# Performance work log

Measured on AMD Instinct MI355X. Metric: run time of the kernel, lower is better.

The kernel has to match this reference:

```python
import jax, jax.numpy as jnp
import numpy as np

TEMP = 0.2
M, K, B = 8192, 128, 100


def setup_inputs() -> dict:
    key = jax.random.key(0)
    k1, k2, k3 = jax.random.split(key, 3)
    f = jax.random.normal(k1, (M, K), dtype=jnp.float32)
    features = f / jnp.linalg.norm(f, axis=1, keepdims=True)
    p = jax.random.normal(k2, (B, K), dtype=jnp.float32)
    protos = p / jnp.linalg.norm(p, axis=1, keepdims=True)
    labels = jax.random.randint(k3, (M,), 0, 2 * B, dtype=jnp.int32)
    proto_labels = jnp.arange(B, dtype=jnp.int32)
    return {"features": features, "labels": labels, "protos": protos, "proto_labels": proto_labels}


def reference(features, labels, protos, proto_labels):
    m = features.shape[0]
    dt = features.dtype
    # base = samples whose label appears among prototype labels
    base = (labels[None, :] == proto_labels[:, None]).any(axis=0)  # [M] bool
    novel = ~base
    nf = novel.astype(dt)
    bf = base.astype(dt)

    S = jnp.matmul(features, features.T) / TEMP          # [M, M] sample-sample logits
    P = jnp.matmul(features, protos.T) / TEMP            # [M, B] sample-proto logits

    # novel-novel pair mask: both novel, off-diagonal (fill_diagonal_(0))
    pair = nf[:, None] * nf[None, :] * (1.0 - jnp.eye(m, dtype=dt))  # [M, M]
    expS = jnp.exp(S)

    # --- novel loss (note: original adds RAW ni_pk.sum, not exp -- faithful) ---
    exp_sum = (expS * pair).sum(axis=1)                  # sum_{j novel, j!=i} exp(S_ij)
    denom = exp_sum + P.sum(axis=1)                      # + raw proto logit sum
    safe_den = jnp.where(novel, denom, 1.0)
    cnt = pair.sum(axis=1)                               # novel_label_mask is all-True 1D -> just pair count
    safe_cnt = jnp.where(cnt > 0, cnt, 1.0)
    # sum_j pair_ij * (S_ij - log(den_i)) = (S*pair).sum - log(den)*cnt
    num = (S * pair).sum(axis=1) - jnp.log(safe_den) * cnt
    loss_novel = (-(num / safe_cnt) * nf).sum()

    # --- base loss ---
    safe_lab = jnp.where(base, labels, 0)
    bi_pi = jnp.take_along_axis(P, safe_lab[:, None], axis=1)[:, 0]  # P[i, labels[i]]
    exp_nk = (expS * nf[None, :]).sum(axis=1)            # sum over novel columns
    exp_pk = jnp.exp(P).sum(axis=1)
    loss_base = (-(bi_pi - jnp.log(exp_nk + exp_pk)) * bf).sum()

    return (loss_novel + loss_base) / m
```

## Files before the change

kernel.cpp:

```cpp
#include <hip/hip_runtime.h>
#include <stdint.h>


#define M_TOT 8192
#define K_DIM 128
#define B_PRO 100
#define INV_T 5.0f
#define C_SCALE 7.2134752044448170f
#define LN2    0.6931471805599453f
#define RT    256
#define NT    (M_TOT / RT)
#define NPAIR (NT * (NT - 1) / 2)
#define NBLK  (NT + NPAIR)
#define BS    136
#define PB    112

#if __has_builtin(__builtin_amdgcn_exp2f)
#define EXP2(x) __builtin_amdgcn_exp2f(x)
#else
#define EXP2(x) __expf((x) * 0.6931471805599453f)
#endif

typedef __attribute__((ext_vector_type(8))) short  short8;
typedef __attribute__((ext_vector_type(4))) float  floatx4;

__device__ __forceinline__ float bf2f(unsigned short u) {
    union { unsigned int i; float f; } v; v.i = ((unsigned int)u) << 16; return v.f;
}
__device__ __forceinline__ unsigned short f2bf(float x) {
    union { float f; unsigned int i; } v; v.f = x;
    return (unsigned short)((v.i + 0x7fffu + ((v.i >> 16) & 1u)) >> 16);
}
__device__ __forceinline__ short8 pack8(float4 a, float4 b) {
    short8 r;
    r[0] = (short)f2bf(a.x); r[1] = (short)f2bf(a.y);
    r[2] = (short)f2bf(a.z); r[3] = (short)f2bf(a.w);
    r[4] = (short)f2bf(b.x); r[5] = (short)f2bf(b.y);
    r[6] = (short)f2bf(b.z); r[7] = (short)f2bf(b.w);
    return r;
}

template<bool DIAG>
__device__ __forceinline__ void sym_body(
        int a, int b, int R0, int C0,
        const float* __restrict__ feat, const int* __restrict__ labels,
        const float* __restrict__ protos, const int* __restrict__ plabels,
        float* __restrict__ rowE,
        int* __restrict__ nfpart, int* __restrict__ nf,
        float* __restrict__ Psum, float* __restrict__ expPsum,
        float* __restrict__ PLab, float* __restrict__ gpart,
        unsigned short* ldsB, float (*colE)[256],
        float* novR, float* novC, int* plabL, int* labRow, float* redD) {
    const int tid = threadIdx.x;
    const int wv = tid >> 6, lane = tid & 63;
    const int quad = lane >> 4, cq = lane & 15;

    if (tid < B_PRO) plabL[tid] = plabels[tid];

    short8 afr[2][4];
    #pragma unroll
    for (int mt = 0; mt < 2; ++mt)
        #pragma unroll
        for (int ks = 0; ks < 4; ++ks) {
            const float* s = feat + (size_t)(R0 + wv * 32 + mt * 16 + cq) * K_DIM
                             + ks * 32 + quad * 8;
            float4 x = ((const float4*)s)[0];
            float4 y = ((const float4*)s)[1];
            afr[mt][ks] = pack8(x, y);
        }
    __syncthreads();

    {
        const int g = (tid < 256) ? (R0 + tid) : (C0 + (tid - 256));
        const int lbl = labels[g];
        int m = 0;
        #pragma unroll 4
        for (int j = 0; j < B_PRO; ++j) m |= (plabL[j] == lbl);
        const float nv = m ? 0.f : 1.f;
        if (tid < 256) { novR[tid] = nv; labRow[tid] = lbl; }
        else novC[tid - 256] = nv;
    }
    __syncthreads();

    float nmR[2][4];
    #pragma unroll
    for (int mt = 0; mt < 2; ++mt)
        #pragma unroll
        for (int r = 0; r < 4; ++r)
            nmR[mt][r] = novR[wv * 32 + mt * 16 + quad * 4 + r];
    float nmcA[16];
    #pragma unroll
    for (int c2 = 0; c2 < 16; ++c2)
        nmcA[c2] = novC[c2 * 16 + cq];

    float accE[2][4];
    #pragma unroll
    for (int mt = 0; mt < 2; ++mt)
        #pragma unroll
        for (int r = 0; r < 4; ++r) accE[mt][r] = 0.f;

    float g_acc = 0.f;

    const int rbase = R0 + wv * 32 + quad * 4;

    #pragma unroll 1
    for (int half = 0; half < 2; ++half) {
        for (int e = tid; e < 2048; e += 512) {
            const int col = e >> 4, sg = e & 15;
            const float* s = feat + (size_t)(C0 + half * 128 + col) * K_DIM + sg * 8;
            float4 x = ((const float4*)s)[0];
            float4 y = ((const float4*)s)[1];
            ushort4 o0 = make_ushort4(f2bf(x.x*C_SCALE), f2bf(x.y*C_SCALE),
                                      f2bf(x.z*C_SCALE), f2bf(x.w*C_SCALE));
            ushort4 o1 = make_ushort4(f2bf(y.x*C_SCALE), f2bf(y.y*C_SCALE),
                                      f2bf(y.z*C_SCALE), f2bf(y.w*C_SCALE));
            *(ushort4*)&ldsB[col * BS + sg * 8]     = o0;
            *(ushort4*)&ldsB[col * BS + sg * 8 + 4] = o1;
        }
        __syncthreads();

        #pragma unroll 2
        for (int ct8 = 0; ct8 < 8; ++ct8) {
            const int ct = half * 8 + ct8;
            const unsigned short* bp = &ldsB[(ct8 * 16 + cq) * BS + quad * 8];
            short8 b0 = *(const short8*)(bp);
            short8 b1 = *(const short8*)(bp + 32);
            short8 b2 = *(const short8*)(bp + 64);
            short8 b3 = *(const short8*)(bp + 96);

            floatx4 D0 = (floatx4){0.f, 0.f, 0.f, 0.f};
            floatx4 D1 = (floatx4){0.f, 0.f, 0.f, 0.f};
            D0 = __builtin_amdgcn_mfma_f32_16x16x32_bf16(afr[0][0], b0, D0, 0, 0, 0);
            D0 = __builtin_amdgcn_mfma_f32_16x16x32_bf16(afr[0][1], b1, D0, 0, 0, 0);
            D0 = __builtin_amdgcn_mfma_f32_16x16x32_bf16(afr[0][2], b2, D0, 0, 0, 0);
            D0 = __builtin_amdgcn_mfma_f32_16x16x32_bf16(afr[0][3], b3, D0, 0, 0, 0);
            D1 = __builtin_amdgcn_mfma_f32_16x16x32_bf16(afr[1][0], b0, D1, 0, 0, 0);
            D1 = __builtin_amdgcn_mfma_f32_16x16x32_bf16(afr[1][1], b1, D1, 0, 0, 0);
            D1 = __builtin_amdgcn_mfma_f32_16x16x32_bf16(afr[1][2], b2, D1, 0, 0, 0);
            D1 = __builtin_amdgcn_mfma_f32_16x16x32_bf16(afr[1][3], b3, D1, 0, 0, 0);

            const float nmc = nmcA[ct];
            float cpE = 0.f;
            #pragma unroll
            for (int r = 0; r < 4; ++r) {
                float e0 = EXP2(D0[r]), e1 = EXP2(D1[r]);
                if (DIAG) {
                    const int colg = C0 + ct * 16 + cq;
                    if (rbase + r == colg) e0 = 0.f;
                    if (rbase + 16 + r == colg) e1 = 0.f;
                }
                accE[0][r] += e0 * nmc;  cpE += e0 * nmR[0][r];
                accE[1][r] += e1 * nmc;  cpE += e1 * nmR[1][r];
            }
            cpE += __shfl_xor(cpE, 16); cpE += __shfl_xor(cpE, 32);
            if (quad == 0) colE[wv][ct * 16 + cq] = cpE;
        }

        if (DIAG && tid < 128) {
            float s = 0.f;
            #pragma unroll 4
            for (int c2 = 0; c2 < 128; ++c2)
                s += novC[half * 128 + c2] * bf2f(ldsB[c2 * BS + tid]);
            g_acc += s;
        }
        __syncthreads();
    }

    #pragma unroll
    for (int mt = 0; mt < 2; ++mt)
        #pragma unroll
        for (int r = 0; r < 4; ++r) {
            float e = accE[mt][r];
            e += __shfl_xor(e, 1); e += __shfl_xor(e, 2);
            e += __shfl_xor(e, 4); e += __shfl_xor(e, 8);
            accE[mt][r] = e;
        }
    if (cq == 0) {
        const size_t slotR = (size_t)b * M_TOT;
        #pragma unroll
        for (int mt = 0; mt < 2; ++mt)
            #pragma unroll
            for (int r = 0; r < 4; ++r) {
                const int rowg = R0 + wv * 32 + mt * 16 + quad * 4 + r;
                rowE[slotR + rowg] = accE[mt][r];
            }
    }

    if (!DIAG) {
        if (tid < 256) {
            float ce = 0.f;
            #pragma unroll
            for (int w = 0; w < 8; ++w) ce += colE[w][tid];
            rowE[(size_t)a * M_TOT + C0 + tid] = ce;
        }
    } else {
        if (tid < 128) gpart[a * 128 + tid] = g_acc;
        {
            float nvv = (tid < 256) ? novR[tid] : 0.f;
            for (int off = 1; off < 64; off <<= 1) nvv += __shfl_xor(nvv, off);
            if (lane == 0) redD[wv] = nvv;
        }
        if (tid < 256) nf[R0 + tid] = (int)novR[tid];

        for (int idx = tid; idx < 3200; idx += 512) {
            const int pr = idx >> 5, sg = idx & 31;
            float4 v = ((const float4*)protos)[idx];
            *(ushort4*)&ldsB[pr * BS + sg * 4] =
                make_ushort4(f2bf(v.x), f2bf(v.y), f2bf(v.z), f2bf(v.w));
        }
        for (int idx = tid; idx < 384; idx += 512) {
            const int pr = B_PRO + (idx >> 5), sg = idx & 31;
            *(ushort4*)&ldsB[pr * BS + sg * 4] = make_ushort4(0, 0, 0, 0);
        }
        __syncthreads();

        if (tid == 0) {
            float c = 0.f;
            #pragma unroll
            for (int w = 0; w < 8; ++w) c += redD[w];
            nfpart[a] = (int)c;
        }

        float ps2[2][4], es2[2][4], pl2[2][4];
        #pragma unroll
        for (int mt = 0; mt < 2; ++mt)
            #pragma unroll
            for (int r = 0; r < 4; ++r) { ps2[mt][r]=0.f; es2[mt][r]=0.f; pl2[mt][r]=0.f; }

        #pragma unroll 1
        for (int g = 0; g < 7; ++g) {
            const unsigned short* bp = &ldsB[(g * 16 + cq) * BS + quad * 8];
            short8 b0 = *(const short8*)(bp);
            short8 b1 = *(const short8*)(bp + 32);
            short8 b2 = *(const short8*)(bp + 64);
            short8 b3 = *(const short8*)(bp + 96);
            floatx4 E0 = (floatx4){0.f, 0.f, 0.f, 0.f};
            floatx4 E1 = (floatx4){0.f, 0.f, 0.f, 0.f};
            E0 = __builtin_amdgcn_mfma_f32_16x16x32_bf16(afr[0][0], b0, E0, 0, 0, 0);
            E0 = __builtin_amdgcn_mfma_f32_16x16x32_bf16(afr[0][1], b1, E0, 0, 0, 0);
            E0 = __builtin_amdgcn_mfma_f32_16x16x32_bf16(afr[0][2], b2, E0, 0, 0, 0);
            E0 = __builtin_amdgcn_mfma_f32_16x16x32_bf16(afr[0][3], b3, E0, 0, 0, 0);
            E1 = __builtin_amdgcn_mfma_f32_16x16x32_bf16(afr[1][0], b0, E1, 0, 0, 0);
            E1 = __builtin_amdgcn_mfma_f32_16x16x32_bf16(afr[1][1], b1, E1, 0, 0, 0);
            E1 = __builtin_amdgcn_mfma_f32_16x16x32_bf16(afr[1][2], b2, E1, 0, 0, 0);
            E1 = __builtin_amdgcn_mfma_f32_16x16x32_bf16(afr[1][3], b3, E1, 0, 0, 0);
            const int bcol = g * 16 + cq;
            if (bcol < B_PRO) {
                #pragma unroll
                for (int r = 0; r < 4; ++r) {
                    const float Pv0 = E0[r] * INV_T;
                    ps2[0][r] += Pv0; es2[0][r] += __expf(Pv0);
                    if (bcol == labRow[wv * 32 + quad * 4 + r]) pl2[0][r] += Pv0;
                    const float Pv1 = E1[r] * INV_T;
                    ps2[1][r] += Pv1; es2[1][r] += __expf(Pv1);
                    if (bcol == labRow[wv * 32 + 16 + quad * 4 + r]) pl2[1][r] += Pv1;
                }
            }
        }
        #pragma unroll
        for (int mt = 0; mt < 2; ++mt)
            #pragma unroll
            for (int r = 0; r < 4; ++r) {
                float p = ps2[mt][r], e = es2[mt][r], l = pl2[mt][r];
                p += __shfl_xor(p, 1); p += __shfl_xor(p, 2);
                p += __shfl_xor(p, 4); p += __shfl_xor(p, 8);
                e += __shfl_xor(e, 1); e += __shfl_xor(e, 2);
                e += __shfl_xor(e, 4); e += __shfl_xor(e, 8);
                l += __shfl_xor(l, 1); l += __shfl_xor(l, 2);
                l += __shfl_xor(l, 4); l += __shfl_xor(l, 8);
                if (cq == 0) {
                    const int rowg = R0 + wv * 32 + mt * 16 + quad * 4 + r;
                    Psum[rowg] = p; expPsum[rowg] = e; PLab[rowg] = l;
                }
            }
    }
}

__global__ __launch_bounds__(512, 4) void k_sym(
        const float* __restrict__ feat, const int* __restrict__ labels,
        const float* __restrict__ protos, const int* __restrict__ plabels,
        float* __restrict__ rowE,
        int* __restrict__ nfpart, int* __restrict__ nf,
        float* __restrict__ Psum, float* __restrict__ expPsum,
        float* __restrict__ PLab, float* __restrict__ gpart,
        float* __restrict__ out) {
    __shared__ unsigned short ldsB[128 * BS];
    __shared__ float colE[8][256];
    __shared__ float novR[256];
    __shared__ float novC[256];
    __shared__ int plabL[B_PRO];
    __shared__ int labRow[256];
    __shared__ float redD[8];

    if (blockIdx.x == 0 && threadIdx.x == 0) out[0] = 0.f;

    const int id = blockIdx.x;
    if (id < NT) {
        sym_body<true>(id, id, id * RT, id * RT,
                       feat, labels, protos, plabels, rowE,
                       nfpart, nf, Psum, expPsum, PLab, gpart,
                       ldsB, colE, novR, novC, plabL, labRow, redD);
    } else {
        const int p = id - NT;
        int aa = 0, rem = p;
        while (rem >= NT - 1 - aa) { rem -= (NT - 1 - aa); ++aa; }
        const int bb2 = aa + 1 + rem;
        sym_body<false>(aa, bb2, aa * RT, bb2 * RT,
                        feat, labels, protos, plabels, rowE,
                        nfpart, nf, Psum, expPsum, PLab, gpart,
                        ldsB, colE, novR, novC, plabL, labRow, redD);
    }
}

__global__ __launch_bounds__(128) void k_final(
        const float* __restrict__ feat,
        const float* __restrict__ rowE,
        const float* __restrict__ Psum, const float* __restrict__ expPsum,
        const float* __restrict__ PLab, const int* __restrict__ nf,
        const int* __restrict__ nfpart, const float* __restrict__ gpart,
        float* __restrict__ out) {
    __shared__ float g[128];
    __shared__ int shNn;
    __shared__ float red[2];
    const int tid = threadIdx.x;
    const int i = blockIdx.x * 128 + tid;

    {
        float s = 0.f;
        #pragma unroll 4
        for (int a2 = 0; a2 < 32; ++a2) s += gpart[a2 * 128 + tid];
        g[tid] = s;
    }
    if (tid < 32) {
        int c = nfpart[tid];
        for (int off = 1; off < 32; off <<= 1) c += __shfl_xor(c, off);
        if (tid == 0) shNn = c;
    }
    __syncthreads();

    float e0 = 0.f, e1 = 0.f, e2 = 0.f, e3 = 0.f;
    #pragma unroll
    for (int s = 0; s < 8; ++s) {
        e0 += rowE[(size_t)(4 * s + 0) * M_TOT + i];
        e1 += rowE[(size_t)(4 * s + 1) * M_TOT + i];
        e2 += rowE[(size_t)(4 * s + 2) * M_TOT + i];
        e3 += rowE[(size_t)(4 * s + 3) * M_TOT + i];
    }
    const float ep = (e0 + e1) + (e2 + e3);

    const float* fr = feat + (size_t)i * K_DIM;
    float sZ = 0.f, dd = 0.f;
    #pragma unroll 8
    for (int k4 = 0; k4 < 32; ++k4) {
        float4 v = ((const float4*)fr)[k4];
        const float fb0 = bf2f(f2bf(v.x)), fc0 = bf2f(f2bf(v.x * C_SCALE));
        const float fb1 = bf2f(f2bf(v.y)), fc1 = bf2f(f2bf(v.y * C_SCALE));
        const float fb2 = bf2f(f2bf(v.z)), fc2 = bf2f(f2bf(v.z * C_SCALE));
        const float fb3 = bf2f(f2bf(v.w)), fc3 = bf2f(f2bf(v.w * C_SCALE));
        const float* gv = &g[k4 * 4];
        sZ += fb0 * gv[0]; dd += fb0 * fc0;
        sZ += fb1 * gv[1]; dd += fb1 * fc1;
        sZ += fb2 * gv[2]; dd += fb2 * fc2;
        sZ += fb3 * gv[3]; dd += fb3 * fc3;
    }

    const int Nn = shNn;
    float contrib;
    if (nf[i]) {
        const float cnt = (float)(Nn - 1);
        const float denom = ep + Psum[i];
        const float sp = sZ - dd;
        const float num = sp * LN2 - logf(denom) * cnt;
        const float sc = cnt > 0.f ? cnt : 1.f;
        contrib = -(num / sc);
    } else {
        contrib = -(PLab[i] - logf(ep + expPsum[i]));
    }
    for (int off = 1; off < 64; off <<= 1) contrib += __shfl_xor(contrib, off);
    if ((tid & 63) == 0) red[tid >> 6] = contrib;
    __syncthreads();
    if (tid == 0) atomicAdd(out, (red[0] + red[1]) * (1.0f / (float)M_TOT));
}

extern "C" void kernel_launch(void* const* d_in, const int* in_sizes, int n_in,
                              void* d_out, int out_size, void* d_ws, size_t ws_size,
                              hipStream_t stream) {
    const float* feat    = (const float*)d_in[0];
    const int*   labels  = (const int*)d_in[1];
    const float* protos  = (const float*)d_in[2];
    const int*   plabels = (const int*)d_in[3];
    float* out = (float*)d_out;

    char* ws = (char*)d_ws;
    float* rowE    = (float*)ws;
    int*   nfpart  = (int*)(ws + 1048576);
    int*   nf      = (int*)(ws + 1052672);
    float* Psum    = (float*)(ws + 1085440);
    float* expPsum = (float*)(ws + 1118208);
    float* PLab    = (float*)(ws + 1150976);
    float* gpart   = (float*)(ws + 1183744);

    k_sym<<<NBLK, 512, 0, stream>>>(feat, labels, protos, plabels,
                                    rowE, nfpart, nf,
                                    Psum, expPsum, PLab, gpart, out);
    k_final<<<64, 128, 0, stream>>>(feat, rowE, Psum, expPsum, PLab,
                                    nf, nfpart, gpart, out);
}
```

Baseline: 102.1 us.

## Split each 256x256 symmetric tile into two 256x128 column-half blocks

Each symmetric tile's work now goes to two blocks, one per 128-column half, instead of one block looping over both halves. This doubles the grid (528 to 1056 blocks) to improve load balance and occupancy across CUs, and removes the in-block serial half loop and its barriers. The cost is that each half-block reloads and repacks the A-row fragments and labels, the rowE and gpart partial buffers double, and k_final must sum twice as many partials. Only the half-0 diagonal blocks compute the prototype logits.

```diff
diff --git a/kernel.cpp b/kernel.cpp
--- a/kernel.cpp
+++ b/kernel.cpp
@@ -11,7 +11,8 @@
 #define RT    256
 #define NT    (M_TOT / RT)
 #define NPAIR (NT * (NT - 1) / 2)
-#define NBLK  (NT + NPAIR)
+#define NTILE (NT + NPAIR)
+#define NBLK  (2 * NTILE)
 #define BS    136
 #define PB    112
 
@@ -42,14 +43,14 @@
 
 template<bool DIAG>
 __device__ __forceinline__ void sym_body(
-        int a, int b, int R0, int C0,
+        int a, int b, int half, int R0, int C0,
         const float* __restrict__ feat, const int* __restrict__ labels,
         const float* __restrict__ protos, const int* __restrict__ plabels,
         float* __restrict__ rowE,
         int* __restrict__ nfpart, int* __restrict__ nf,
         float* __restrict__ Psum, float* __restrict__ expPsum,
         float* __restrict__ PLab, float* __restrict__ gpart,
-        unsigned short* ldsB, float (*colE)[256],
+        unsigned short* ldsB, float (*colE)[128],
         float* novR, float* novC, int* plabL, int* labRow, float* redD) {
     const int tid = threadIdx.x;
     const int wv = tid >> 6, lane = tid & 63;
@@ -68,9 +69,22 @@
             float4 y = ((const float4*)s)[1];
             afr[mt][ks] = pack8(x, y);
         }
+
+    for (int e = tid; e < 2048; e += 512) {
+        const int col = e >> 4, sg = e & 15;
+        const float* s = feat + (size_t)(C0 + col) * K_DIM + sg * 8;
+        float4 x = ((const float4*)s)[0];
+        float4 y = ((const float4*)s)[1];
+        ushort4 o0 = make_ushort4(f2bf(x.x*C_SCALE), f2bf(x.y*C_SCALE),
+                                  f2bf(x.z*C_SCALE), f2bf(x.w*C_SCALE));
+        ushort4 o1 = make_ushort4(f2bf(y.x*C_SCALE), f2bf(y.y*C_SCALE),
+                                  f2bf(y.z*C_SCALE), f2bf(y.w*C_SCALE));
+        *(ushort4*)&ldsB[col * BS + sg * 8]     = o0;
+        *(ushort4*)&ldsB[col * BS + sg * 8 + 4] = o1;
+    }
     __syncthreads();
 
-    {
+    if (tid < 384) {
         const int g = (tid < 256) ? (R0 + tid) : (C0 + (tid - 256));
         const int lbl = labels[g];
         int m = 0;
@@ -88,9 +102,9 @@
         #pragma unroll
         for (int r = 0; r < 4; ++r)
             nmR[mt][r] = novR[wv * 32 + mt * 16 + quad * 4 + r];
-    float nmcA[16];
-    #pragma unroll
-    for (int c2 = 0; c2 < 16; ++c2)
+    float nmcA[8];
+    #pragma unroll
+    for (int c2 = 0; c2 < 8; ++c2)
         nmcA[c2] = novC[c2 * 16 + cq];
 
     float accE[2][4];
@@ -99,71 +113,49 @@
         #pragma unroll
         for (int r = 0; r < 4; ++r) accE[mt][r] = 0.f;
 
+    const int rbase = R0 + wv * 32 + quad * 4;
+
+    #pragma unroll 2
+    for (int ct = 0; ct < 8; ++ct) {
+        const unsigned short* bp = &ldsB[(ct * 16 + cq) * BS + quad * 8];
+        short8 b0 = *(const short8*)(bp);
+        short8 b1 = *(const short8*)(bp + 32);
+        short8 b2 = *(const short8*)(bp + 64);
+        short8 b3 = *(const short8*)(bp + 96);
+
+        floatx4 D0 = (floatx4){0.f, 0.f, 0.f, 0.f};
+        floatx4 D1 = (floatx4){0.f, 0.f, 0.f, 0.f};
+        D0 = __builtin_amdgcn_mfma_f32_16x16x32_bf16(afr[0][0], b0, D0, 0, 0, 0);
+        D0 = __builtin_amdgcn_mfma_f32_16x16x32_bf16(afr[0][1], b1, D0, 0, 0, 0);
+        D0 = __builtin_amdgcn_mfma_f32_16x16x32_bf16(afr[0][2], b2, D0, 0, 0, 0);
+        D0 = __builtin_amdgcn_mfma_f32_16x16x32_bf16(afr[0][3], b3, D0, 0, 0, 0);
+        D1 = __builtin_amdgcn_mfma_f32_16x16x32_bf16(afr[1][0], b0, D1, 0, 0, 0);
+        D1 = __builtin_amdgcn_mfma_f32_16x16x32_bf16(afr[1][1], b1, D1, 0, 0, 0);
+        D1 = __builtin_amdgcn_mfma_f32_16x16x32_bf16(afr[1][2], b2, D1, 0, 0, 0);
+        D1 = __builtin_amdgcn_mfma_f32_16x16x32_bf16(afr[1][3], b3, D1, 0, 0, 0);
+
+        const float nmc = nmcA[ct];
+        float cpE = 0.f;
+        #pragma unroll
+        for (int r = 0; r < 4; ++r) {
+            float e0 = EXP2(D0[r]), e1 = EXP2(D1[r]);
+            if (DIAG) {
+                const int colg = C0 + ct * 16 + cq;
+                if (rbase + r == colg) e0 = 0.f;
+                if (rbase + 16 + r == colg) e1 = 0.f;
+            }
+            accE[0][r] += e0 * nmc;  cpE += e0 * nmR[0][r];
+            accE[1][r] += e1 * nmc;  cpE += e1 * nmR[1][r];
+        }
+        cpE += __shfl_xor(cpE, 16); cpE += __shfl_xor(cpE, 32);
+        if (quad == 0) colE[wv][ct * 16 + cq] = cpE;
+    }
+
     float g_acc = 0.f;
-
-    const int rbase = R0 + wv * 32 + quad * 4;
-
-    #pragma unroll 1
-    for (int half = 0; half < 2; ++half) {
-        for (int e = tid; e < 2048; e += 512) {
-            const int col = e >> 4, sg = e & 15;
-            const float* s = feat + (size_t)(C0 + half * 128 + col) * K_DIM + sg * 8;
-            float4 x = ((const float4*)s)[0];
-            float4 y = ((const float4*)s)[1];
-            ushort4 o0 = make_ushort4(f2bf(x.x*C_SCALE), f2bf(x.y*C_SCALE),
-                                      f2bf(x.z*C_SCALE), f2bf(x.w*C_SCALE));
-            ushort4 o1 = make_ushort4(f2bf(y.x*C_SCALE), f2bf(y.y*C_SCALE),
-                                      f2bf(y.z*C_SCALE), f2bf(y.w*C_SCALE));
-            *(ushort4*)&ldsB[col * BS + sg * 8]     = o0;
-            *(ushort4*)&ldsB[col * BS + sg * 8 + 4] = o1;
-        }
-        __syncthreads();
-
-        #pragma unroll 2
-        for (int ct8 = 0; ct8 < 8; ++ct8) {
-            const int ct = half * 8 + ct8;
-            const unsigned short* bp = &ldsB[(ct8 * 16 + cq) * BS + quad * 8];
-            short8 b0 = *(const short8*)(bp);
-            short8 b1 = *(const short8*)(bp + 32);
-            short8 b2 = *(const short8*)(bp + 64);
-            short8 b3 = *(const short8*)(bp + 96);
-
-            floatx4 D0 = (floatx4){0.f, 0.f, 0.f, 0.f};
-            floatx4 D1 = (floatx4){0.f, 0.f, 0.f, 0.f};
-            D0 = __builtin_amdgcn_mfma_f32_16x16x32_bf16(afr[0][0], b0, D0, 0, 0, 0);
-            D0 = __builtin_amdgcn_mfma_f32_16x16x32_bf16(afr[0][1], b1, D0, 0, 0, 0);
-            D0 = __builtin_amdgcn_mfma_f32_16x16x32_bf16(afr[0][2], b2, D0, 0, 0, 0);
-            D0 = __builtin_amdgcn_mfma_f32_16x16x32_bf16(afr[0][3], b3, D0, 0, 0, 0);
-            D1 = __builtin_amdgcn_mfma_f32_16x16x32_bf16(afr[1][0], b0, D1, 0, 0, 0);
-            D1 = __builtin_amdgcn_mfma_f32_16x16x32_bf16(afr[1][1], b1, D1, 0, 0, 0);
-            D1 = __builtin_amdgcn_mfma_f32_16x16x32_bf16(afr[1][2], b2, D1, 0, 0, 0);
-            D1 = __builtin_amdgcn_mfma_f32_16x16x32_bf16(afr[1][3], b3, D1, 0, 0, 0);
-
-            const float nmc = nmcA[ct];
-            float cpE = 0.f;
-            #pragma unroll
-            for (int r = 0; r < 4; ++r) {
-                float e0 = EXP2(D0[r]), e1 = EXP2(D1[r]);
-                if (DIAG) {
-                    const int colg = C0 + ct * 16 + cq;
-                    if (rbase + r == colg) e0 = 0.f;
-                    if (rbase + 16 + r == colg) e1 = 0.f;
-                }
-                accE[0][r] += e0 * nmc;  cpE += e0 * nmR[0][r];
-                accE[1][r] += e1 * nmc;  cpE += e1 * nmR[1][r];
-            }
-            cpE += __shfl_xor(cpE, 16); cpE += __shfl_xor(cpE, 32);
-            if (quad == 0) colE[wv][ct * 16 + cq] = cpE;
-        }
-
-        if (DIAG && tid < 128) {
-            float s = 0.f;
-            #pragma unroll 4
-            for (int c2 = 0; c2 < 128; ++c2)
-                s += novC[half * 128 + c2] * bf2f(ldsB[c2 * BS + tid]);
-            g_acc += s;
-        }
-        __syncthreads();
+    if (DIAG && tid < 128) {
+        #pragma unroll 4
+        for (int c2 = 0; c2 < 128; ++c2)
+            g_acc += novC[c2] * bf2f(ldsB[c2 * BS + tid]);
     }
 
     #pragma unroll
@@ -176,7 +168,7 @@
             accE[mt][r] = e;
         }
     if (cq == 0) {
-        const size_t slotR = (size_t)b * M_TOT;
+        const size_t slotR = (size_t)(2 * b + half) * M_TOT;
         #pragma unroll
         for (int mt = 0; mt < 2; ++mt)
             #pragma unroll
@@ -186,93 +178,98 @@
             }
     }
 
+    __syncthreads();
+
     if (!DIAG) {
-        if (tid < 256) {
+        if (tid < 128) {
             float ce = 0.f;
             #pragma unroll
             for (int w = 0; w < 8; ++w) ce += colE[w][tid];
-            rowE[(size_t)a * M_TOT + C0 + tid] = ce;
+            rowE[(size_t)(2 * a + half) * M_TOT + C0 + tid] = ce;
         }
     } else {
-        if (tid < 128) gpart[a * 128 + tid] = g_acc;
-        {
-            float nvv = (tid < 256) ? novR[tid] : 0.f;
-            for (int off = 1; off < 64; off <<= 1) nvv += __shfl_xor(nvv, off);
-            if (lane == 0) redD[wv] = nvv;
-        }
-        if (tid < 256) nf[R0 + tid] = (int)novR[tid];
-
-        for (int idx = tid; idx < 3200; idx += 512) {
-            const int pr = idx >> 5, sg = idx & 31;
-            float4 v = ((const float4*)protos)[idx];
-            *(ushort4*)&ldsB[pr * BS + sg * 4] =
-                make_ushort4(f2bf(v.x), f2bf(v.y), f2bf(v.z), f2bf(v.w));
-        }
-        for (int idx = tid; idx < 384; idx += 512) {
-            const int pr = B_PRO + (idx >> 5), sg = idx & 31;
-            *(ushort4*)&ldsB[pr * BS + sg * 4] = make_ushort4(0, 0, 0, 0);
-        }
-        __syncthreads();
-
-        if (tid == 0) {
-            float c = 0.f;
+        if (tid < 128) gpart[(2 * a + half) * 128 + tid] = g_acc;
+
+        if (half == 0) {
+            {
+                float nvv = (tid < 256) ? novR[tid] : 0.f;
+                for (int off = 1; off < 64; off <<= 1) nvv += __shfl_xor(nvv, off);
+                if (lane == 0) redD[wv] = nvv;
+            }
+            if (tid < 256) nf[R0 + tid] = (int)novR[tid];
+
+            for (int idx = tid; idx < 3200; idx += 512) {
+                const int pr = idx >> 5, sg = idx & 31;
+                float4 v = ((const float4*)protos)[idx];
+                *(ushort4*)&ldsB[pr * BS + sg * 4] =
+                    make_ushort4(f2bf(v.x), f2bf(v.y), f2bf(v.z), f2bf(v.w));
+            }
+            for (int idx = tid; idx < 384; idx += 512) {
+                const int pr = B_PRO + (idx >> 5), sg = idx & 31;
+                *(ushort4*)&ldsB[pr * BS + sg * 4] = make_ushort4(0, 0, 0, 0);
+            }
+            __syncthreads();
+
+            if (tid == 0) {
+                float c = 0.f;
+                #pragma unroll
+                for (int w = 0; w < 8; ++w) c += redD[w];
+                nfpart[a] = (int)c;
+            }
+
+            float ps2[2][4], es2[2][4], pl2[2][4];
             #pragma unroll
-            for (int w = 0; w < 8; ++w) c += redD[w];
-            nfpart[a] = (int)c;
-        }
-
-        float ps2[2][4], es2[2][4], pl2[2][4];
-        #pragma unroll
-        for (int mt = 0; mt < 2; ++mt)
+            for (int mt = 0; mt < 2; ++mt)
+                #pragma unroll
+                for (int r = 0; r < 4; ++r) { ps2[mt][r]=0.f; es2[mt][r]=0.f; pl2[mt][r]=0.f; }
+
+            #pragma unroll 1
+            for (int g = 0; g < 7; ++g) {
+                const unsigned short* bp = &ldsB[(g * 16 + cq) * BS + quad * 8];
+                short8 b0 = *(const short8*)(bp);
+                short8 b1 = *(const short8*)(bp + 32);
+                short8 b2 = *(const short8*)(bp + 64);
+                short8 b3 = *(const short8*)(bp + 96);
+                floatx4 E0 = (floatx4){0.f, 0.f, 0.f, 0.f};
+                floatx4 E1 = (floatx4){0.f, 0.f, 0.f, 0.f};
+                E0 = __builtin_amdgcn_mfma_f32_16x16x32_bf16(afr[0][0], b0, E0, 0, 0, 0);
+                E0 = __builtin_amdgcn_mfma_f32_16x16x32_bf16(afr[0][1], b1, E0, 0, 0, 0);
+                E0 = __builtin_amdgcn_mfma_f32_16x16x32_bf16(afr[0][2], b2, E0, 0, 0, 0);
+                E0 = __builtin_amdgcn_mfma_f32_16x16x32_bf16(afr[0][3], b3, E0, 0, 0, 0);
+                E1 = __builtin_amdgcn_mfma_f32_16x16x32_bf16(afr[1][0], b0, E1, 0, 0, 0);
+                E1 = __builtin_amdgcn_mfma_f32_16x16x32_bf16(afr[1][1], b1, E1, 0, 0, 0);
+                E1 = __builtin_amdgcn_mfma_f32_16x16x32_bf16(afr[1][2], b2, E1, 0, 0, 0);
+                E1 = __builtin_amdgcn_mfma_f32_16x16x32_bf16(afr[1][3], b3, E1, 0, 0, 0);
+                const int bcol = g * 16 + cq;
+                if (bcol < B_PRO) {
+                    #pragma unroll
+                    for (int r = 0; r < 4; ++r) {
+                        const float Pv0 = E0[r] * INV_T;
+                        ps2[0][r] += Pv0; es2[0][r] += __expf(Pv0);
+                        if (bcol == labRow[wv * 32 + quad * 4 + r]) pl2[0][r] += Pv0;
+                        const float Pv1 = E1[r] * INV_T;
+                        ps2[1][r] += Pv1; es2[1][r] += __expf(Pv1);
+                        if (bcol == labRow[wv * 32 + 16 + quad * 4 + r]) pl2[1][r] += Pv1;
+                    }
+                }
+            }
             #pragma unroll
-            for (int r = 0; r < 4; ++r) { ps2[mt][r]=0.f; es2[mt][r]=0.f; pl2[mt][r]=0.f; }
-
-        #pragma unroll 1
-        for (int g = 0; g < 7; ++g) {
-            const unsigned short* bp = &ldsB[(g * 16 + cq) * BS + quad * 8];
-            short8 b0 = *(const short8*)(bp);
-            short8 b1 = *(const short8*)(bp + 32);
-            short8 b2 = *(const short8*)(bp + 64);
-            short8 b3 = *(const short8*)(bp + 96);
-            floatx4 E0 = (floatx4){0.f, 0.f, 0.f, 0.f};
-            floatx4 E1 = (floatx4){0.f, 0.f, 0.f, 0.f};
-            E0 = __builtin_amdgcn_mfma_f32_16x16x32_bf16(afr[0][0], b0, E0, 0, 0, 0);
-            E0 = __builtin_amdgcn_mfma_f32_16x16x32_bf16(afr[0][1], b1, E0, 0, 0, 0);
-            E0 = __builtin_amdgcn_mfma_f32_16x16x32_bf16(afr[0][2], b2, E0, 0, 0, 0);
-            E0 = __builtin_amdgcn_mfma_f32_16x16x32_bf16(afr[0][3], b3, E0, 0, 0, 0);
-            E1 = __builtin_amdgcn_mfma_f32_16x16x32_bf16(afr[1][0], b0, E1, 0, 0, 0);
-            E1 = __builtin_amdgcn_mfma_f32_16x16x32_bf16(afr[1][1], b1, E1, 0, 0, 0);
-            E1 = __builtin_amdgcn_mfma_f32_16x16x32_bf16(afr[1][2], b2, E1, 0, 0, 0);
-            E1 = __builtin_amdgcn_mfma_f32_16x16x32_bf16(afr[1][3], b3, E1, 0, 0, 0);
-            const int bcol = g * 16 + cq;
-            if (bcol < B_PRO) {
+            for (int mt = 0; mt < 2; ++mt)
                 #pragma unroll
                 for (int r = 0; r < 4; ++r) {
-                    const float Pv0 = E0[r] * INV_T;
-                    ps2[0][r] += Pv0; es2[0][r] += __expf(Pv0);
-                    if (bcol == labRow[wv * 32 + quad * 4 + r]) pl2[0][r] += Pv0;
-                    const float Pv1 = E1[r] * INV_T;
-                    ps2[1][r] += Pv1; es2[1][r] += __expf(Pv1);
-                    if (bcol == labRow[wv * 32 + 16 + quad * 4 + r]) pl2[1][r] += Pv1;
+                    float p = ps2[mt][r], e = es2[mt][r], l = pl2[mt][r];
+                    p += __shfl_xor(p, 1); p += __shfl_xor(p, 2);
+                    p += __shfl_xor(p, 4); p += __shfl_xor(p, 8);
+                    e += __shfl_xor(e, 1); e += __shfl_xor(e, 2);
+                    e += __shfl_xor(e, 4); e += __shfl_xor(e, 8);
+                    l += __shfl_xor(l, 1); l += __shfl_xor(l, 2);
+                    l += __shfl_xor(l, 4); l += __shfl_xor(l, 8);
+                    if (cq == 0) {
+                        const int rowg = R0 + wv * 32 + mt * 16 + quad * 4 + r;
+                        Psum[rowg] = p; expPsum[rowg] = e; PLab[rowg] = l;
+                    }
                 }
-            }
         }
-        #pragma unroll
-        for (int mt = 0; mt < 2; ++mt)
-            #pragma unroll
-            for (int r = 0; r < 4; ++r) {
-                float p = ps2[mt][r], e = es2[mt][r], l = pl2[mt][r];
-                p += __shfl_xor(p, 1); p += __shfl_xor(p, 2);
-                p += __shfl_xor(p, 4); p += __shfl_xor(p, 8);
-                e += __shfl_xor(e, 1); e += __shfl_xor(e, 2);
-                e += __shfl_xor(e, 4); e += __shfl_xor(e, 8);
-                l += __shfl_xor(l, 1); l += __shfl_xor(l, 2);
-                l += __shfl_xor(l, 4); l += __shfl_xor(l, 8);
-                if (cq == 0) {
-                    const int rowg = R0 + wv * 32 + mt * 16 + quad * 4 + r;
-                    Psum[rowg] = p; expPsum[rowg] = e; PLab[rowg] = l;
-                }
-            }
     }
 }
 
@@ -285,27 +282,28 @@
         float* __restrict__ PLab, float* __restrict__ gpart,
         float* __restrict__ out) {
     __shared__ unsigned short ldsB[128 * BS];
-    __shared__ float colE[8][256];
+    __shared__ float colE[8][128];
     __shared__ float novR[256];
-    __shared__ float novC[256];
+    __shared__ float novC[128];
     __shared__ int plabL[B_PRO];
     __shared__ int labRow[256];
     __shared__ float redD[8];
 
     if (blockIdx.x == 0 && threadIdx.x == 0) out[0] = 0.f;
 
-    const int id = blockIdx.x;
-    if (id < NT) {
-        sym_body<true>(id, id, id * RT, id * RT,
+    const int tile = blockIdx.x >> 1, half = blockIdx.x & 1;
+    if (tile < NT) {
+        const int c = tile;
+        sym_body<true>(c, c, half, c * RT, c * RT + half * 128,
                        feat, labels, protos, plabels, rowE,
                        nfpart, nf, Psum, expPsum, PLab, gpart,
                        ldsB, colE, novR, novC, plabL, labRow, redD);
     } else {
-        const int p = id - NT;
+        const int p = tile - NT;
         int aa = 0, rem = p;
         while (rem >= NT - 1 - aa) { rem -= (NT - 1 - aa); ++aa; }
         const int bb2 = aa + 1 + rem;
-        sym_body<false>(aa, bb2, aa * RT, bb2 * RT,
+        sym_body<false>(aa, bb2, half, aa * RT, bb2 * RT + half * 128,
                         feat, labels, protos, plabels, rowE,
                         nfpart, nf, Psum, expPsum, PLab, gpart,
                         ldsB, colE, novR, novC, plabL, labRow, redD);
@@ -328,7 +326,7 @@
     {
         float s = 0.f;
         #pragma unroll 4
-        for (int a2 = 0; a2 < 32; ++a2) s += gpart[a2 * 128 + tid];
+        for (int a2 = 0; a2 < 64; ++a2) s += gpart[a2 * 128 + tid];
         g[tid] = s;
     }
     if (tid < 32) {
@@ -340,7 +338,7 @@
 
     float e0 = 0.f, e1 = 0.f, e2 = 0.f, e3 = 0.f;
     #pragma unroll
-    for (int s = 0; s < 8; ++s) {
+    for (int s = 0; s < 16; ++s) {
         e0 += rowE[(size_t)(4 * s + 0) * M_TOT + i];
         e1 += rowE[(size_t)(4 * s + 1) * M_TOT + i];
         e2 += rowE[(size_t)(4 * s + 2) * M_TOT + i];
@@ -393,12 +391,12 @@
 
     char* ws = (char*)d_ws;
     float* rowE    = (float*)ws;
-    int*   nfpart  = (int*)(ws + 1048576);
-    int*   nf      = (int*)(ws + 1052672);
-    float* Psum    = (float*)(ws + 1085440);
-    float* expPsum = (float*)(ws + 1118208);
-    float* PLab    = (float*)(ws + 1150976);
-    float* gpart   = (float*)(ws + 1183744);
+    int*   nfpart  = (int*)(ws + 2097152);
+    int*   nf      = (int*)(ws + 2101248);
+    float* Psum    = (float*)(ws + 2134016);
+    float* expPsum = (float*)(ws + 2166784);
+    float* PLab    = (float*)(ws + 2199552);
+    float* gpart   = (float*)(ws + 2232320);
 
     k_sym<<<NBLK, 512, 0, stream>>>(feat, labels, protos, plabels,
                                     rowE, nfpart, nf,
```

After: 110.4 us. 1.08x slower.
